# Kernel tuning notes

Hardware: AMD Instinct MI355X
Metric: run time of the kernel (lower is better)

## Reference

```python
import jax, jax.numpy as jnp
import numpy as np

HIDDEN = 1024
HEADS = 16
HEAD_DIM = HIDDEN // HEADS  # 64
RP_DIM = 256
KERNEL_EPS = 1e-3


def _gaussian_orthogonal_matrix(nb_rows, nb_cols, seed=0):
    """Orthogonal random features (scaling=0), as in Performer FAVOR+."""
    rng = np.random.RandomState(seed)
    blocks = []
    n_full = nb_rows // nb_cols
    for _ in range(n_full):
        q, _ = np.linalg.qr(rng.randn(nb_cols, nb_cols))
        blocks.append(q.T)
    rem = nb_rows - n_full * nb_cols
    if rem > 0:
        q, _ = np.linalg.qr(rng.randn(nb_cols, nb_cols))
        blocks.append(q.T[:rem])
    mat = np.concatenate(blocks, axis=0)
    # scaling=0: row norms drawn from chi distribution (norms of gaussian rows)
    multiplier = np.linalg.norm(rng.randn(nb_rows, nb_cols), axis=1)
    return (multiplier[:, None] * mat).astype(np.float32)


def setup_inputs() -> dict:
    key = jax.random.key(0)
    kx, kw = jax.random.split(key)
    x = jax.random.normal(kx, (4, 4096, HIDDEN), dtype=jnp.float32)
    w_qkv = jax.random.normal(kw, (HIDDEN, 3 * HIDDEN), dtype=jnp.float32) * 0.02
    b_qkv = jnp.zeros((3 * HIDDEN,), dtype=jnp.float32)
    proj = jnp.asarray(_gaussian_orthogonal_matrix(RP_DIM, HEAD_DIM))  # [M, Dh]
    return {"x": x, "w_qkv": w_qkv, "b_qkv": b_qkv, "proj": proj}


def reference(x, w_qkv, b_qkv, proj):
    B, N, _ = x.shape
    qkv = x @ w_qkv + b_qkv  # [B, N, 3*hidden]
    q, k, v = jnp.split(qkv, 3, axis=-1)

    def to_heads(t):
        return t.reshape(B, N, HEADS, HEAD_DIM).transpose(0, 2, 1, 3)  # bhnd

    q, k, v = to_heads(q), to_heads(k), to_heads(v)

    # forward scales by d**-0.25, generalized_kernel normalizes by d**-0.25 again
    scale = HEAD_DIM ** -0.5
    # generalized kernel features: relu(x_norm @ proj^T) + eps  -> [B,H,N,M]
    q_prime = jax.nn.relu(jnp.einsum('bhnd,md->bhnm', q * scale, proj)) + KERNEL_EPS
    k_prime = jax.nn.relu(jnp.einsum('bhnd,md->bhnm', k * scale, proj)) + KERNEL_EPS

    # non-causal linear attention
    k_sum = k_prime.sum(axis=2)  # [B,H,M]
    d_inv = 1.0 / jnp.einsum('bhnm,bhm->bhn', q_prime, k_sum)  # [B,H,N]
    context = jnp.einsum('bhnm,bhnd->bhmd', k_prime, v)  # [B,H,M,Dh]
    out = jnp.einsum('bhmd,bhnm,bhn->bhnd', context, q_prime, d_inv)

    out = out.transpose(0, 2, 1, 3).reshape(B, N, HIDDEN)
    return out
```

## Files before the change

### kernel.cpp

```cpp
#include <hip/hip_runtime.h>

#define B_   4
#define N_   4096
#define NH   16
#define DH   64
#define HID  1024
#define NC3  3072
#define M_   256
#define BH   64
#define SCALE 0.125f
#define EPS   1e-3f
#define CH2  8
#define CH3  16

typedef _Float16 half8  __attribute__((ext_vector_type(8)));
typedef _Float16 half4v __attribute__((ext_vector_type(4)));
typedef float floatx4   __attribute__((ext_vector_type(4)));

#define GLD_LDS16(gptr, lds_base) \
  __builtin_amdgcn_global_load_lds((const __attribute__((address_space(1))) void*)(gptr), \
                                   (__attribute__((address_space(3))) void*)(lds_base), 16, 0, 0)

__global__ __launch_bounds__(256) void convert_xh(
    const float* __restrict__ x, _Float16* __restrict__ xh)
{
    const size_t i = ((size_t)blockIdx.x * 256 + threadIdx.x) * 8;
    float4 a = *(const float4*)(x + i);
    float4 b = *(const float4*)(x + i + 4);
    half8 h;
    h[0] = (_Float16)a.x; h[1] = (_Float16)a.y; h[2] = (_Float16)a.z; h[3] = (_Float16)a.w;
    h[4] = (_Float16)b.x; h[5] = (_Float16)b.y; h[6] = (_Float16)b.z; h[7] = (_Float16)b.w;
    *(half8*)(xh + i) = h;
}

__global__ __launch_bounds__(256) void convert_wT(
    const float* __restrict__ w, _Float16* __restrict__ wT)
{
    __shared__ float t[64][65];
    const int tid = threadIdx.x;
    const int kb = blockIdx.y * 64, nb = blockIdx.x * 64;
    const int c = tid & 63, r0 = tid >> 6;
#pragma unroll
    for (int rr = 0; rr < 64; rr += 4)
        t[rr + r0][c] = w[(size_t)(kb + rr + r0) * NC3 + nb + c];
    __syncthreads();
    const float sc = (nb < 2048) ? SCALE : 1.0f;
#pragma unroll
    for (int rr = 0; rr < 64; rr += 4)
        wT[(size_t)(nb + rr + r0) * HID + kb + c] = (_Float16)(t[c][rr + r0] * sc);
}

__global__ __launch_bounds__(256) void convert_projh(
    const float* __restrict__ proj, _Float16* __restrict__ projh)
{
    const int i = blockIdx.x * 256 + threadIdx.x;
    projh[i] = (_Float16)proj[i];
}

__global__ __launch_bounds__(256) void gemm_qkv_mfma(
    const _Float16* __restrict__ xh, const _Float16* __restrict__ wT,
    const float* __restrict__ bias,
    _Float16* __restrict__ qh, _Float16* __restrict__ kh, _Float16* __restrict__ vTh)
{
    __shared__ __align__(16) _Float16 As[128 * 32];
    __shared__ __align__(16) _Float16 Bs[128 * 32];

    const int tid  = threadIdx.x;
    const int lane = tid & 63;
    const int wv   = tid >> 6;
    const int row0 = blockIdx.y * 128;
    const int col0 = blockIdx.x * 128;

    const int wm = (wv & 1) * 64;
    const int wn = (wv >> 1) * 64;
    const int lr = lane & 15;
    const int lg = lane >> 4;

    const int s_r = lane >> 2;
    const int s_q = lane & 3;

    floatx4 acc[4][4] = {};

    for (int k0 = 0; k0 < HID; k0 += 32) {
#pragma unroll
        for (int s = 0; s < 2; ++s) {
            const int R = wv * 32 + s * 16;
            const int r = R + s_r;
            const int qd = s_q ^ ((r >> 1) & 3);
            GLD_LDS16(xh + (size_t)(row0 + r) * HID + k0 + 8 * qd, (char*)As + R * 64);
        }
#pragma unroll
        for (int s = 0; s < 2; ++s) {
            const int R = wv * 32 + s * 16;
            const int r = R + s_r;
            const int qd = s_q ^ ((r >> 1) & 3);
            GLD_LDS16(wT + (size_t)(col0 + r) * HID + k0 + 8 * qd, (char*)Bs + R * 64);
        }
        __syncthreads();

        half8 af[4], bf[4];
#pragma unroll
        for (int i = 0; i < 4; ++i) {
            const int m = wm + 16 * i + lr;
            const int p = lg ^ ((m >> 1) & 3);
            af[i] = *(const half8*)((const char*)As + m * 64 + p * 16);
        }
#pragma unroll
        for (int j = 0; j < 4; ++j) {
            const int n = wn + 16 * j + lr;
            const int p = lg ^ ((n >> 1) & 3);
            bf[j] = *(const half8*)((const char*)Bs + n * 64 + p * 16);
        }
#pragma unroll
        for (int i = 0; i < 4; ++i)
#pragma unroll
            for (int j = 0; j < 4; ++j)
                acc[i][j] = __builtin_amdgcn_mfma_f32_16x16x32_f16(af[i], bf[j], acc[i][j], 0, 0, 0);
        __syncthreads();
    }

#pragma unroll
    for (int j = 0; j < 4; ++j) {
        const int col = col0 + wn + 16 * j + lr;
        const int which = col >> 10;
        const int h = (col >> 6) & 15;
        const int d = col & 63;
        const float bb = bias[col] * ((which < 2) ? SCALE : 1.0f);
        if (which == 2) {
#pragma unroll
            for (int i = 0; i < 4; ++i) {
                const int m0 = row0 + wm + 16 * i + 4 * lg;
                const int bi = m0 >> 12, n0 = m0 & (N_ - 1);
                half4v hv;
#pragma unroll
                for (int rg = 0; rg < 4; ++rg) hv[rg] = (_Float16)(acc[i][j][rg] + bb);
                *(half4v*)(vTh + ((size_t)(bi * NH + h) * DH + d) * N_ + n0) = hv;
            }
        } else {
            _Float16* dst = (which == 0) ? qh : kh;
#pragma unroll
            for (int i = 0; i < 4; ++i)
#pragma unroll
                for (int rg = 0; rg < 4; ++rg) {
                    const int m = row0 + wm + 16 * i + 4 * lg + rg;
                    const int bi = m >> 12, n = m & (N_ - 1);
                    dst[((size_t)(bi * NH + h) * N_ + n) * DH + d] =
                        (_Float16)(acc[i][j][rg] + bb);
                }
        }
    }
}

__global__ __launch_bounds__(256) void kv_ctx_mfma(
    const _Float16* __restrict__ kh, const _Float16* __restrict__ vTh,
    const _Float16* __restrict__ projh,
    float* __restrict__ ctx_part, float* __restrict__ ksum_part)
{
    __shared__ __align__(16) _Float16 Kt[64 * 64];
    __shared__ __align__(16) _Float16 Vt[64 * 64];
    __shared__ __align__(16) _Float16 Sp[256 * 64];

    const int tid  = threadIdx.x;
    const int lane = tid & 63;
    const int wv   = tid >> 6;
    const int lr = lane & 15, lg = lane >> 4;
    const int bh = blockIdx.y, chunk = blockIdx.x;
    const int n_base = chunk * (N_ / CH2);

    half8 bfP[4][2];
#pragma unroll
    for (int j = 0; j < 4; ++j)
#pragma unroll
        for (int ks = 0; ks < 2; ++ks)
            bfP[j][ks] = *(const half8*)(projh + (size_t)(64 * wv + 16 * j + lr) * DH + 32 * ks + 8 * lg);

    floatx4 cacc[4][4] = {};
    float ks_acc[4] = {0.f, 0.f, 0.f, 0.f};

    for (int t = 0; t < (N_ / CH2) / 64; ++t) {
        const int n0 = n_base + t * 64;
        __syncthreads();
#pragma unroll
        for (int s = 0; s < 2; ++s) {
            const int R = wv * 16 + s * 8;
            const int r = R + (lane >> 3);
            const int db = (lane & 7) ^ (r & 7);
            GLD_LDS16(kh + ((size_t)(bh * N_ + n0 + r)) * DH + db * 8, (char*)Kt + R * 128);
        }
#pragma unroll
        for (int s = 0; s < 2; ++s) {
            const int R = wv * 16 + s * 8;
            const int r = R + (lane >> 3);
            const int db = (lane & 7) ^ (r & 7);
            GLD_LDS16(vTh + ((size_t)(bh * DH + r)) * N_ + n0 + db * 8, (char*)Vt + R * 128);
        }
        __syncthreads();

        floatx4 s[4][4] = {};
#pragma unroll
        for (int ks = 0; ks < 2; ++ks) {
            half8 aK[4];
#pragma unroll
            for (int i = 0; i < 4; ++i) {
                const int r = 16 * i + lr;
                aK[i] = *(const half8*)((const char*)Kt + r * 128 + (((4 * ks + lg) ^ (r & 7)) * 16));
            }
#pragma unroll
            for (int i = 0; i < 4; ++i)
#pragma unroll
                for (int j = 0; j < 4; ++j)
                    s[i][j] = __builtin_amdgcn_mfma_f32_16x16x32_f16(aK[i], bfP[j][ks], s[i][j], 0, 0, 0);
        }
#pragma unroll
        for (int i = 0; i < 4; ++i)
#pragma unroll
            for (int j = 0; j < 4; ++j) {
                const int m = 64 * wv + 16 * j + lr;
                const int nn0 = 16 * i + 4 * lg;
                half4v h4;
#pragma unroll
                for (int rg = 0; rg < 4; ++rg) {
                    const float kv = fmaxf(s[i][j][rg], 0.f) + EPS;
                    ks_acc[j] += kv;
                    h4[rg] = (_Float16)kv;
                }
                const int db = nn0 >> 3, sub = nn0 & 7;
                *(half4v*)((char*)Sp + m * 128 + ((db ^ (m & 7)) * 16) + sub * 2) = h4;
            }
#pragma unroll
        for (int ks = 0; ks < 2; ++ks) {
            half8 aV[4], bS[4];
#pragma unroll
            for (int i = 0; i < 4; ++i) {
                const int r = 16 * i + lr;
                aV[i] = *(const half8*)((const char*)Vt + r * 128 + (((4 * ks + lg) ^ (r & 7)) * 16));
            }
#pragma unroll
            for (int j = 0; j < 4; ++j) {
                const int m = 64 * wv + 16 * j + lr;
                bS[j] = *(const half8*)((const char*)Sp + m * 128 + (((4 * ks + lg) ^ (m & 7)) * 16));
            }
#pragma unroll
            for (int i = 0; i < 4; ++i)
#pragma unroll
                for (int j = 0; j < 4; ++j)
                    cacc[i][j] = __builtin_amdgcn_mfma_f32_16x16x32_f16(aV[i], bS[j], cacc[i][j], 0, 0, 0);
        }
    }

#pragma unroll
    for (int i = 0; i < 4; ++i)
#pragma unroll
        for (int j = 0; j < 4; ++j)
#pragma unroll
            for (int rg = 0; rg < 4; ++rg) {
                const int d = 16 * i + 4 * lg + rg;
                const int m = 64 * wv + 16 * j + lr;
                ctx_part[(((size_t)chunk * BH + bh) * DH + d) * M_ + m] = cacc[i][j][rg];
            }
#pragma unroll
    for (int j = 0; j < 4; ++j) {
        float v = ks_acc[j];
        v += __shfl_xor(v, 16);
        v += __shfl_xor(v, 32);
        if (lg == 0)
            ksum_part[((size_t)chunk * BH + bh) * M_ + 64 * wv + 16 * j + lr] = v;
    }
}

__global__ __launch_bounds__(256) void reduce_ctx(
    const float* __restrict__ ctx_part, const float* __restrict__ ksum_part,
    _Float16* __restrict__ ctxTh, _Float16* __restrict__ ksumh)
{
    const int idx = blockIdx.x * 256 + threadIdx.x;
    const int CTX = BH * DH * M_;
    if (idx < CTX) {
        float sum = 0.f;
#pragma unroll
        for (int c = 0; c < CH2; ++c) sum += ctx_part[(size_t)c * CTX + idx];
        ctxTh[idx] = (_Float16)sum;
    } else {
        const int kidx = idx - CTX;
        if (kidx < BH * M_) {
            float sum = 0.f;
#pragma unroll
            for (int c = 0; c < CH2; ++c) sum += ksum_part[(size_t)c * BH * M_ + kidx];
            ksumh[kidx] = (_Float16)sum;
        }
    }
}

__global__ __launch_bounds__(256) void attn_out_mfma(
    const _Float16* __restrict__ qh, const _Float16* __restrict__ projh,
    const _Float16* __restrict__ ctxTh, const _Float16* __restrict__ ksumh,
    float* __restrict__ out)
{
    __shared__ __align__(16) _Float16 Sp[64 * 256];

    const int tid  = threadIdx.x;
    const int lane = tid & 63;
    const int wv   = tid >> 6;
    const int lr = lane & 15, lg = lane >> 4;
    const int bh = blockIdx.y;
    const int bi = bh >> 4, h = bh & 15;
    const int n_base = blockIdx.x * (N_ / CH3);

    half8 afP[4][2];
#pragma unroll
    for (int I = 0; I < 4; ++I)
#pragma unroll
        for (int ks = 0; ks < 2; ++ks)
            afP[I][ks] = *(const half8*)(projh + (size_t)(64 * wv + 16 * I + lr) * DH + 32 * ks + 8 * lg);

    for (int t = 0; t < (N_ / CH3) / 64; ++t) {
        const int n0 = n_base + t * 64;
        __syncthreads();
        floatx4 sacc[4][4] = {};
#pragma unroll
        for (int ks = 0; ks < 2; ++ks) {
            half8 bq[4];
#pragma unroll
            for (int J = 0; J < 4; ++J)
                bq[J] = *(const half8*)(qh + ((size_t)bh * N_ + n0 + 16 * J + lr) * DH + 32 * ks + 8 * lg);
#pragma unroll
            for (int I = 0; I < 4; ++I)
#pragma unroll
                for (int J = 0; J < 4; ++J)
                    sacc[I][J] = __builtin_amdgcn_mfma_f32_16x16x32_f16(afP[I][ks], bq[J], sacc[I][J], 0, 0, 0);
        }
#pragma unroll
        for (int I = 0; I < 4; ++I)
#pragma unroll
            for (int J = 0; J < 4; ++J) {
                const int n = 16 * J + lr;
                const int m0 = 64 * wv + 16 * I + 4 * lg;
                half4v h4;
#pragma unroll
                for (int rg = 0; rg < 4; ++rg)
                    h4[rg] = (_Float16)(fmaxf(sacc[I][J][rg], 0.f) + EPS);
                const int db = m0 >> 3, sub = m0 & 7;
                *(half4v*)((char*)Sp + n * 512 + ((db ^ (n & 31)) * 16) + sub * 2) = h4;
            }
        __syncthreads();
        floatx4 oacc[4] = {};
        floatx4 dacc = {};
        const int nl = 16 * wv + lr;
#pragma unroll
        for (int ks = 0; ks < 8; ++ks) {
            half8 aq = *(const half8*)((const char*)Sp + nl * 512 + (((4 * ks + lg) ^ (nl & 31)) * 16));
#pragma unroll
            for (int j = 0; j < 4; ++j) {
                half8 bc = *(const half8*)(ctxTh + ((size_t)bh * DH + 16 * j + lr) * M_ + 32 * ks + 8 * lg);
                oacc[j] = __builtin_amdgcn_mfma_f32_16x16x32_f16(aq, bc, oacc[j], 0, 0, 0);
            }
            half8 bk = {};
            if (lr == 0)
                bk = *(const half8*)(ksumh + (size_t)bh * M_ + 32 * ks + 8 * lg);
            dacc = __builtin_amdgcn_mfma_f32_16x16x32_f16(aq, bk, dacc, 0, 0, 0);
        }
#pragma unroll
        for (int rg = 0; rg < 4; ++rg) {
            float den = dacc[rg];
            den = __shfl(den, lane & 48);
            const float dinv = 1.f / den;
            const int n = n0 + 16 * wv + 4 * lg + rg;
#pragma unroll
            for (int j = 0; j < 4; ++j)
                out[(((size_t)bi * N_ + n) * NH + h) * DH + 16 * j + lr] = oacc[j][rg] * dinv;
        }
    }
}

extern "C" void kernel_launch(void* const* d_in, const int* in_sizes, int n_in,
                              void* d_out, int out_size, void* d_ws, size_t ws_size,
                              hipStream_t stream) {
    const float* x    = (const float*)d_in[0];
    const float* w    = (const float*)d_in[1];
    const float* bias = (const float*)d_in[2];
    const float* proj = (const float*)d_in[3];
    float* out = (float*)d_out;
    char* ws = (char*)d_ws;

    const size_t XN  = (size_t)B_ * N_ * HID;
    const size_t QKV = (size_t)BH * N_ * DH;
    const size_t CTX = (size_t)BH * DH * M_;

    _Float16* xh       = (_Float16*)ws;                          ws += XN * 2;
    _Float16* wT       = (_Float16*)ws;                          ws += NC3 * HID * 2;
    _Float16* projh    = (_Float16*)ws;                          ws += M_ * DH * 2;
    _Float16* qh       = (_Float16*)ws;                          ws += QKV * 2;
    _Float16* kh       = (_Float16*)ws;                          ws += QKV * 2;
    _Float16* vTh      = (_Float16*)ws;                          ws += QKV * 2;
    _Float16* ctxTh    = (_Float16*)ws;                          ws += CTX * 2;
    _Float16* ksumh    = (_Float16*)ws;                          ws += BH * M_ * 2;
    float*    ctx_part = (float*)ws;                             ws += (size_t)CH2 * CTX * 4;
    float*    ksum_part= (float*)ws;                             ws += (size_t)CH2 * BH * M_ * 4;

    convert_xh<<<dim3(XN / (256 * 8)), 256, 0, stream>>>(x, xh);
    convert_wT<<<dim3(NC3 / 64, HID / 64), 256, 0, stream>>>(w, wT);
    convert_projh<<<dim3(M_ * DH / 256), 256, 0, stream>>>(proj, projh);

    gemm_qkv_mfma<<<dim3(NC3 / 128, (B_ * N_) / 128), 256, 0, stream>>>(xh, wT, bias, qh, kh, vTh);

    kv_ctx_mfma<<<dim3(CH2, BH), 256, 0, stream>>>(kh, vTh, projh, ctx_part, ksum_part);

    reduce_ctx<<<dim3((CTX + BH * M_ + 255) / 256), 256, 0, stream>>>(ctx_part, ksum_part, ctxTh, ksumh);

    attn_out_mfma<<<dim3(CH3, BH), 256, 0, stream>>>(qh, projh, ctxTh, ksumh, out);
}
```

Baseline: 380.0 us.

## Restructure QKV GEMM into 256x256 double-buffered pipelined tiles with XCD-aware mapping

The QKV projection GEMM moves from 128x128 tiles with K=32 steps to 256x256 tiles with K=64 steps, using 512 threads, a 128KB double-buffered LDS, and manual vmcnt/barrier scheduling that prefetches two K-tiles ahead. It adds an XOR swizzle, setprio around the MFMA bursts, and a block-to-tile remapping meant to group tiles per XCD for better L2 reuse. The goal is to raise MFMA utilization and hide global load latency in the dominant GEMM. The cost is much higher register and LDS use, which limits occupancy, and fragile hand-written wait counts.

```diff
diff --git a/kernel.cpp b/kernel.cpp
--- a/kernel.cpp
+++ b/kernel.cpp
@@ -57,95 +57,157 @@
     projh[i] = (_Float16)proj[i];
 }
 
-__global__ __launch_bounds__(256) void gemm_qkv_mfma(
+__device__ __forceinline__ void stage_tile_qkv(
+    const _Float16* __restrict__ xh, const _Float16* __restrict__ wT,
+    int row0, int col0, int kt, char* ab, char* bb, int wv, int srow, int sblk)
+{
+    const size_t ko = (size_t)kt * 64;
+#pragma unroll
+    for (int s = 0; s < 4; ++s) {
+        const int r = s * 64 + srow;
+        GLD_LDS16(xh + (size_t)(row0 + r) * HID + ko + 8 * sblk, ab + s * 8192 + wv * 1024);
+        GLD_LDS16(wT + (size_t)(col0 + r) * HID + ko + 8 * sblk, bb + s * 8192 + wv * 1024);
+    }
+}
+
+__global__ __launch_bounds__(512, 2) void gemm_qkv_mfma(
     const _Float16* __restrict__ xh, const _Float16* __restrict__ wT,
     const float* __restrict__ bias,
     _Float16* __restrict__ qh, _Float16* __restrict__ kh, _Float16* __restrict__ vTh)
 {
-    __shared__ __align__(16) _Float16 As[128 * 32];
-    __shared__ __align__(16) _Float16 Bs[128 * 32];
+    __shared__ __align__(16) char smem[131072];
 
     const int tid  = threadIdx.x;
     const int lane = tid & 63;
     const int wv   = tid >> 6;
-    const int row0 = blockIdx.y * 128;
-    const int col0 = blockIdx.x * 128;
-
-    const int wm = (wv & 1) * 64;
-    const int wn = (wv >> 1) * 64;
-    const int lr = lane & 15;
-    const int lg = lane >> 4;
-
-    const int s_r = lane >> 2;
-    const int s_q = lane & 3;
-
-    floatx4 acc[4][4] = {};
-
-    for (int k0 = 0; k0 < HID; k0 += 32) {
-#pragma unroll
-        for (int s = 0; s < 2; ++s) {
-            const int R = wv * 32 + s * 16;
-            const int r = R + s_r;
-            const int qd = s_q ^ ((r >> 1) & 3);
-            GLD_LDS16(xh + (size_t)(row0 + r) * HID + k0 + 8 * qd, (char*)As + R * 64);
-        }
-#pragma unroll
-        for (int s = 0; s < 2; ++s) {
-            const int R = wv * 32 + s * 16;
-            const int r = R + s_r;
-            const int qd = s_q ^ ((r >> 1) & 3);
-            GLD_LDS16(wT + (size_t)(col0 + r) * HID + k0 + 8 * qd, (char*)Bs + R * 64);
-        }
-        __syncthreads();
+    const int wm   = wv >> 2;
+    const int wn   = wv & 3;
+    const int lr   = lane & 15;
+    const int lg   = lane >> 4;
+    const int lr7  = lr & 7;
+
+    const int bid  = blockIdx.x;
+    const int tile = ((bid & 7) * 96) + (bid >> 3);
+    const int tm   = tile / 12;
+    const int tn   = tile - tm * 12;
+    const int row0 = tm * 256;
+    const int col0 = tn * 256;
+
+    const int srow = 8 * wv + (lane >> 3);
+    const int sblk = (lane & 7) ^ (lane >> 3);
+
+    char* buf0A = smem;
+    char* buf0B = smem + 32768;
+    char* buf1A = smem + 65536;
+    char* buf1B = smem + 98304;
+
+    floatx4 acc[8][4] = {};
+
+    stage_tile_qkv(xh, wT, row0, col0, 0, buf0A, buf0B, wv, srow, sblk);
+    stage_tile_qkv(xh, wT, row0, col0, 1, buf1A, buf1B, wv, srow, sblk);
+
+    for (int t = 0; t < 16; ++t) {
+        if (t < 15) asm volatile("s_waitcnt vmcnt(8)" ::: "memory");
+        else        asm volatile("s_waitcnt vmcnt(0)" ::: "memory");
+        __builtin_amdgcn_s_barrier();
+        __builtin_amdgcn_sched_barrier(0);
+
+        char* ab = (t & 1) ? buf1A : buf0A;
+        char* bb = (t & 1) ? buf1B : buf0B;
 
         half8 af[4], bf[4];
-#pragma unroll
-        for (int i = 0; i < 4; ++i) {
-            const int m = wm + 16 * i + lr;
-            const int p = lg ^ ((m >> 1) & 3);
-            af[i] = *(const half8*)((const char*)As + m * 64 + p * 16);
-        }
-#pragma unroll
-        for (int j = 0; j < 4; ++j) {
-            const int n = wn + 16 * j + lr;
-            const int p = lg ^ ((n >> 1) & 3);
-            bf[j] = *(const half8*)((const char*)Bs + n * 64 + p * 16);
-        }
+
+#pragma unroll
+        for (int i = 0; i < 4; ++i)
+            af[i] = *(const half8*)(ab + (wm * 128 + 16 * i + lr) * 128 + ((lg ^ lr7) * 16));
+#pragma unroll
+        for (int j = 0; j < 4; ++j)
+            bf[j] = *(const half8*)(bb + (wn * 64 + 16 * j + lr) * 128 + ((lg ^ lr7) * 16));
+        __builtin_amdgcn_s_setprio(1);
 #pragma unroll
         for (int i = 0; i < 4; ++i)
 #pragma unroll
             for (int j = 0; j < 4; ++j)
                 acc[i][j] = __builtin_amdgcn_mfma_f32_16x16x32_f16(af[i], bf[j], acc[i][j], 0, 0, 0);
-        __syncthreads();
+        __builtin_amdgcn_s_setprio(0);
+        __builtin_amdgcn_s_barrier();
+        __builtin_amdgcn_sched_barrier(0);
+
+#pragma unroll
+        for (int i = 0; i < 4; ++i)
+            af[i] = *(const half8*)(ab + (wm * 128 + 16 * (4 + i) + lr) * 128 + ((lg ^ lr7) * 16));
+        __builtin_amdgcn_s_setprio(1);
+#pragma unroll
+        for (int i = 0; i < 4; ++i)
+#pragma unroll
+            for (int j = 0; j < 4; ++j)
+                acc[4 + i][j] = __builtin_amdgcn_mfma_f32_16x16x32_f16(af[i], bf[j], acc[4 + i][j], 0, 0, 0);
+        __builtin_amdgcn_s_setprio(0);
+        __builtin_amdgcn_s_barrier();
+        __builtin_amdgcn_sched_barrier(0);
+
+#pragma unroll
+        for (int i = 0; i < 4; ++i)
+            af[i] = *(const half8*)(ab + (wm * 128 + 16 * i + lr) * 128 + (((4 + lg) ^ lr7) * 16));
+#pragma unroll
+        for (int j = 0; j < 4; ++j)
+            bf[j] = *(const half8*)(bb + (wn * 64 + 16 * j + lr) * 128 + (((4 + lg) ^ lr7) * 16));
+        __builtin_amdgcn_s_setprio(1);
+#pragma unroll
+        for (int i = 0; i < 4; ++i)
+#pragma unroll
+            for (int j = 0; j < 4; ++j)
+                acc[i][j] = __builtin_amdgcn_mfma_f32_16x16x32_f16(af[i], bf[j], acc[i][j], 0, 0, 0);
+        __builtin_amdgcn_s_setprio(0);
+        __builtin_amdgcn_s_barrier();
+        __builtin_amdgcn_sched_barrier(0);
+
+#pragma unroll
+        for (int i = 0; i < 4; ++i)
+            af[i] = *(const half8*)(ab + (wm * 128 + 16 * (4 + i) + lr) * 128 + (((4 + lg) ^ lr7) * 16));
+        asm volatile("s_waitcnt lgkmcnt(0)" ::: "memory");
+        __builtin_amdgcn_sched_barrier(0);
+        __builtin_amdgcn_s_barrier();
+        __builtin_amdgcn_sched_barrier(0);
+        if (t < 14)
+            stage_tile_qkv(xh, wT, row0, col0, t + 2, ab, bb, wv, srow, sblk);
+        __builtin_amdgcn_sched_barrier(0);
+        __builtin_amdgcn_s_setprio(1);
+#pragma unroll
+        for (int i = 0; i < 4; ++i)
+#pragma unroll
+            for (int j = 0; j < 4; ++j)
+                acc[4 + i][j] = __builtin_amdgcn_mfma_f32_16x16x32_f16(af[i], bf[j], acc[4 + i][j], 0, 0, 0);
+        __builtin_amdgcn_s_setprio(0);
     }
 
 #pragma unroll
     for (int j = 0; j < 4; ++j) {
-        const int col = col0 + wn + 16 * j + lr;
+        const int col = col0 + wn * 64 + 16 * j + lr;
         const int which = col >> 10;
         const int h = (col >> 6) & 15;
         const int d = col & 63;
-        const float bb = bias[col] * ((which < 2) ? SCALE : 1.0f);
+        const float bb2 = bias[col] * ((which < 2) ? SCALE : 1.0f);
         if (which == 2) {
 #pragma unroll
-            for (int i = 0; i < 4; ++i) {
-                const int m0 = row0 + wm + 16 * i + 4 * lg;
+            for (int i = 0; i < 8; ++i) {
+                const int m0 = row0 + wm * 128 + 16 * i + 4 * lg;
                 const int bi = m0 >> 12, n0 = m0 & (N_ - 1);
                 half4v hv;
 #pragma unroll
-                for (int rg = 0; rg < 4; ++rg) hv[rg] = (_Float16)(acc[i][j][rg] + bb);
+                for (int rg = 0; rg < 4; ++rg) hv[rg] = (_Float16)(acc[i][j][rg] + bb2);
                 *(half4v*)(vTh + ((size_t)(bi * NH + h) * DH + d) * N_ + n0) = hv;
             }
         } else {
             _Float16* dst = (which == 0) ? qh : kh;
 #pragma unroll
-            for (int i = 0; i < 4; ++i)
+            for (int i = 0; i < 8; ++i)
 #pragma unroll
                 for (int rg = 0; rg < 4; ++rg) {
-                    const int m = row0 + wm + 16 * i + 4 * lg + rg;
+                    const int m = row0 + wm * 128 + 16 * i + 4 * lg + rg;
                     const int bi = m >> 12, n = m & (N_ - 1);
                     dst[((size_t)(bi * NH + h) * N_ + n) * DH + d] =
-                        (_Float16)(acc[i][j][rg] + bb);
+                        (_Float16)(acc[i][j][rg] + bb2);
                 }
         }
     }
@@ -400,7 +462,7 @@
     convert_wT<<<dim3(NC3 / 64, HID / 64), 256, 0, stream>>>(w, wT);
     convert_projh<<<dim3(M_ * DH / 256), 256, 0, stream>>>(proj, projh);
 
-    gemm_qkv_mfma<<<dim3(NC3 / 128, (B_ * N_) / 128), 256, 0, stream>>>(xh, wT, bias, qh, kh, vTh);
+    gemm_qkv_mfma<<<dim3(768), dim3(512), 0, stream>>>(xh, wT, bias, qh, kh, vTh);
 
     kv_ctx_mfma<<<dim3(CH2, BH), 256, 0, stream>>>(kh, vTh, projh, ctx_part, ksum_part);
 
```

New measurement: 367.7 us. -3.2%, faster.
